# Kernel optimization log

Measured on AMD Instinct MI355X. Metric: run time of the kernel, lower is better.

Reference implementation:

```python
import jax, jax.numpy as jnp
import numpy as np

B, N, D, DS, LAT, FD, NF = 2, 384, 128, 3, 256, 1, 2
NPOS = DS * (2 * 5 + 1)  # 3 + 3*2*5 = 33
FREQS = np.linspace(1.0, 32.0, 5)  # torch.linspace(1, 2**5, 5)
EPS = 1e-5


def _bn(x, g, b):
    # BatchNorm1d, train-mode batch stats: normalize per channel over (batch, points)
    m = jnp.mean(x, axis=(0, 1))
    v = jnp.var(x, axis=(0, 1))
    return (x - m) * jax.lax.rsqrt(v + EPS) * g + b


def _tblock(xyz4, f, Wq, Wk, Wv, Wg1, bg1, Wg2, bg2, Wpe, bpe, g, b):
    # group_all=True full vector attention. f: [B,n,D], xyz4: [B,n,3]
    q = f @ Wq.T
    k = f @ Wk.T
    v = f @ Wv.T
    # knn_xyz gathered under no_grad in torch -> stop_gradient on the key side
    pd = xyz4[:, :, None] - jax.lax.stop_gradient(xyz4)[:, None]  # [B,n,n,3]
    parts = [pd]
    for fr in FREQS:
        parts.append(jnp.sin(pd * fr))
        parts.append(jnp.cos(pd * fr))
    pos = jnp.concatenate(parts, axis=-1) @ Wpe.T + bpe  # [B,n,n,D]
    edges = q[:, :, None] - k[:, None] + pos  # [B,n,n,D]
    h = jax.nn.relu(edges @ Wg1.T + bg1)
    attn = jax.nn.softmax(h @ Wg2.T + bg2, axis=-2)  # softmax over neighbor axis
    res = jnp.sum(attn * (v[:, None] + pos), axis=2)  # einsum bmnf,bmnf->bmf
    return _bn(res + f, g, b)


def setup_inputs() -> dict:
    key = jax.random.key(0)
    ks = iter(jax.random.split(key, 40))
    def rn(shape, s=0.05):
        return jax.random.normal(next(ks), shape, dtype=jnp.float32) * s
    z = lambda *s: jnp.zeros(s, jnp.float32)
    o = lambda *s: jnp.ones(s, jnp.float32)
    nb = NF + 1  # begin block + nfinal blocks
    return {
        "xyz": jax.random.normal(next(ks), (B, N, DS), dtype=jnp.float32),
        "feats": jax.random.normal(next(ks), (B, N, FD), dtype=jnp.float32),
        "enc_W": rn((D, FD)), "enc_b": z(D),
        "tb_Wq": rn((nb, D, D)), "tb_Wk": rn((nb, D, D)), "tb_Wv": rn((nb, D, D)),
        "tb_Wg1": rn((nb, D, D)), "tb_bg1": z(nb, D),
        "tb_Wg2": rn((nb, D, D)), "tb_bg2": z(nb, D),
        "tb_Wpe": rn((nb, D, NPOS)), "tb_bpe": z(nb, D),
        "tb_gamma": o(nb, D), "tb_beta": z(nb, D),
        "em_W1": rn((NF, D, D)), "em_b1": z(NF, D),
        "em_W2": rn((NF, D, D)), "em_b2": z(NF, D),
        "em_gamma": o(NF, D), "em_beta": z(NF, D),
        "fcf_W1": rn((LAT, D)), "fcf_b1": z(LAT),
        "fcf_W2": rn((LAT, LAT)), "fcf_b2": z(LAT),
    }


def reference(xyz, feats, enc_W, enc_b, tb_Wq, tb_Wk, tb_Wv, tb_Wg1, tb_bg1,
              tb_Wg2, tb_bg2, tb_Wpe, tb_bpe, tb_gamma, tb_beta,
              em_W1, em_b1, em_W2, em_b2, em_gamma, em_beta,
              fcf_W1, fcf_b1, fcf_W2, fcf_b2):
    f = feats @ enc_W.T + enc_b  # enc_feats
    x4 = xyz * 4.0
    for i in range(NF + 1):  # i=0: transformer_begin; i>=1: final transformers
        f = _tblock(x4, f, tb_Wq[i], tb_Wk[i], tb_Wv[i], tb_Wg1[i], tb_bg1[i],
                    tb_Wg2[i], tb_bg2[i], tb_Wpe[i], tb_bpe[i], tb_gamma[i], tb_beta[i])
        if i > 0:
            j = i - 1  # ElementwiseMLP: bn(x + relu(conv2(relu(conv1(x)))))
            y = jax.nn.relu(f @ em_W1[j].T + em_b1[j])
            y = jax.nn.relu(y @ em_W2[j].T + em_b2[j])
            f = _bn(f + y, em_gamma[j], em_beta[j])
    e = jax.nn.relu(f @ fcf_W1.T + fcf_b1) @ fcf_W2.T + fcf_b2
    return jnp.max(e, axis=1)  # lat_rep [B, lat_dim]
```

## Files before the change

### kernel.cpp

```cpp
#include <hip/hip_runtime.h>
#include <hip/hip_bf16.h>

#define B_ 2
#define N_ 384
#define D_ 128
#define LAT_ 256
#define NPOS_ 33
#define ROWS_ (B_*N_)
#define NT_ 64
#define ITERS_ (N_/NT_)

typedef __attribute__((ext_vector_type(8))) short bf16x8;
typedef __attribute__((ext_vector_type(4))) float f32x4;

#define MFMA(a,b,c) __builtin_amdgcn_mfma_f32_16x16x32_bf16((a),(b),(c),0,0,0)

__device__ __forceinline__ unsigned short f2bf(float x) {
    unsigned int u = __float_as_uint(x);
    u += 0x7FFFu + ((u >> 16) & 1u);
    return (unsigned short)(u >> 16);
}
__device__ __forceinline__ float bf2f(unsigned short u) {
    return __uint_as_float(((unsigned int)u) << 16);
}

__device__ __forceinline__ float bn_apply(float x, const float* stats, const float* gam,
                                          const float* bet, int d) {
    float s  = stats[d], sq = stats[128 + d];
    float mean = s * (1.f/ROWS_);
    float var  = sq * (1.f/ROWS_) - mean*mean;
    return (x - mean) * rsqrtf(var + 1e-5f) * gam[d] + bet[d];
}

#define PB_FPREP 192
#define PB_PSI   (PB_FPREP + 51)
#define PB_ENC   (PB_PSI + 384)
#define PB_WQG   (PB_ENC + 384)
__global__ __launch_bounds__(256) void prep_kernel(
    const float* __restrict__ xyz, const float* __restrict__ feats,
    const float* __restrict__ enc_W, const float* __restrict__ enc_b,
    const float* __restrict__ Wg1, const float* __restrict__ Wpe, const float* __restrict__ bpe,
    const float* __restrict__ Wq, const float* __restrict__ Wk,
    unsigned short* __restrict__ gF, float* __restrict__ psi,
    float* __restrict__ wqg, float* __restrict__ wkg, float* __restrict__ f)
{
    const int blk = blockIdx.x, t = threadIdx.x;
    if (blk < PB_FPREP) {
        int i = blk*256 + t;
        int n = i >> 6, q = i & 63;
        float val;
        if (q == 0) val = 1.f;
        else if (q < 4) val = 4.f*xyz[n*3 + (q-1)];
        else if (q < 34) {
            int u = q-4, fi = u/6, rem = u - fi*6, j = rem >> 1;
            const float fr = fi==0?1.f:(fi==1?8.75f:(fi==2?16.5f:(fi==3?24.25f:32.f)));
            float a = fr*4.f*xyz[n*3+j];
            val = (rem & 1) ? __sinf(a) : __cosf(a);
        } else val = 0.f;
        gF[n*64 + (q ^ ((n & 7) << 3))] = f2bf(val);
    } else if (blk < PB_PSI) {
        __shared__ float col2[2][D_];
        const int colid = (blk - PB_FPREP)*2 + (t >> 7);
        const int layer = colid / 34, p = colid - layer*34;
        const int e = t & 127, half = t >> 7;
        col2[half][e] = (p < NPOS_) ? Wpe[layer*D_*NPOS_ + e*NPOS_ + p]
                                    : bpe[layer*D_ + e];
        __syncthreads();
        const float* wg1 = Wg1 + layer*D_*D_;
        float acc = 0.f;
        #pragma unroll 4
        for (int d4 = 0; d4 < 32; ++d4) {
            float4 w = *(const float4*)(wg1 + e*D_ + d4*4);
            acc += w.x*col2[half][d4*4] + w.y*col2[half][d4*4+1]
                 + w.z*col2[half][d4*4+2] + w.w*col2[half][d4*4+3];
        }
        psi[layer*D_*34 + e*34 + p] = acc;
    } else if (blk < PB_ENC) {
        int i = (blk - PB_PSI)*256 + t;
        int r = i >> 7, d = i & 127;
        f[i] = feats[r]*enc_W[d] + enc_b[d];
    } else {
        __shared__ float col2[2][D_];
        const int colid = (blk - PB_ENC)*2 + (t >> 7);
        const int layer = colid >> 8, rem = colid & 255;
        const int mat = rem >> 7, ecol = rem & 127;
        const int e = t & 127, half = t >> 7;
        const float* Wsrc = mat ? Wk : Wq;
        col2[half][e] = Wsrc[layer*D_*D_ + e*D_ + ecol];
        __syncthreads();
        const float* wg1 = Wg1 + layer*D_*D_;
        float acc = 0.f;
        #pragma unroll 4
        for (int d4 = 0; d4 < 32; ++d4) {
            float4 w = *(const float4*)(wg1 + e*D_ + d4*4);
            acc += w.x*col2[half][d4*4] + w.y*col2[half][d4*4+1]
                 + w.z*col2[half][d4*4+2] + w.w*col2[half][d4*4+3];
        }
        float* dst = mat ? wkg : wqg;
        dst[layer*D_*D_ + e*D_ + ecol] = acc;
    }
}

__global__ __launch_bounds__(128) void qkv3_kernel(const float* __restrict__ graw,
    const float* __restrict__ stats, const float* __restrict__ gam, const float* __restrict__ bet,
    int use_stats,
    const float* __restrict__ Wv, const float* __restrict__ Wqg, const float* __restrict__ Wkg,
    const float* __restrict__ bg1,
    float* __restrict__ hb, unsigned short* __restrict__ kw16, unsigned short* __restrict__ v16)
{
    __shared__ float row[D_];
    const int r = blockIdx.x, d = threadIdx.x;
    float x = graw[r*D_ + d];
    if (use_stats) x = bn_apply(x, stats, gam, bet, d);
    row[d] = x;
    __syncthreads();
    float av = 0.f, ah = bg1[d], ak = 0.f;
    #pragma unroll 4
    for (int e4 = 0; e4 < D_/4; ++e4) {
        float4 wv = *(const float4*)(Wv  + d*D_ + e4*4);
        float4 wh = *(const float4*)(Wqg + d*D_ + e4*4);
        float4 wk = *(const float4*)(Wkg + d*D_ + e4*4);
        float4 xx = *(const float4*)&row[e4*4];
        av += wv.x*xx.x + wv.y*xx.y + wv.z*xx.z + wv.w*xx.w;
        ah += wh.x*xx.x + wh.y*xx.y + wh.z*xx.z + wh.w*xx.w;
        ak += wk.x*xx.x + wk.y*xx.y + wk.z*xx.z + wk.w*xx.w;
    }
    v16[r*D_ + d]  = f2bf(av);
    hb[r*D_ + d]   = ah;
    kw16[r*D_ + d] = f2bf(ak);
}

__global__ __launch_bounds__(512) void attn_mfma_kernel(
    const float* __restrict__ xyz, const float* __restrict__ graw,
    const float* __restrict__ stats_in, const float* __restrict__ gam_in,
    const float* __restrict__ bet_in, int use_stats,
    const float* __restrict__ hbb,
    const unsigned short* __restrict__ kwb, const unsigned short* __restrict__ vb,
    const unsigned short* __restrict__ gF,
    const float* __restrict__ psiL,
    const float* __restrict__ Wpe, const float* __restrict__ bpe,
    const float* __restrict__ Wg2, const float* __restrict__ bg2,
    float* __restrict__ gout, float* __restrict__ stats_out)
{
    __shared__ unsigned short sF[NT_*64];
    __shared__ unsigned short sH[NT_*128];
    __shared__ float sRed[4*128];

    const int t   = threadIdx.x;
    const int w   = t >> 6;
    const int l   = t & 63;
    const int lr  = l & 15;
    const int lg  = l >> 4;
    const int rb2 = w >> 2;
    const int ct0 = (w & 3) * 2;

    const int row  = blockIdx.x;
    const int b    = row / N_;
    const int brow = b * N_;

    uint4 freg = *(const uint4*)(gF + (size_t)brow*64 + t*8);
    unsigned short kw_us[2][2][4];
    unsigned short v_us[2][2][4];
    auto loadKW = [&](int n0) {
        #pragma unroll
        for (int rt = 0; rt < 2; ++rt)
        #pragma unroll
        for (int ct = 0; ct < 2; ++ct) {
            const int d = (ct0 + ct)*16 + lr;
            #pragma unroll
            for (int r = 0; r < 4; ++r) {
                const int rr = rb2*32 + rt*16 + lg*4 + r;
                kw_us[rt][ct][r] = kwb[(brow + n0 + rr)*D_ + d];
            }
        }
    };
    auto loadV = [&](int n0) {
        #pragma unroll
        for (int rt = 0; rt < 2; ++rt)
        #pragma unroll
        for (int ct = 0; ct < 2; ++ct) {
            const int d = (ct0 + ct)*16 + lr;
            #pragma unroll
            for (int r = 0; r < 4; ++r) {
                const int rr = rb2*32 + rt*16 + lg*4 + r;
                v_us[rt][ct][r] = vb[(brow + n0 + rr)*D_ + d];
            }
        }
    };
    loadKW(0);

    bf16x8 bWg2[2][4], bG[2][2], bT[2][2];
    float  hb_c[2], bg2_c[2];

    const float xm0 = 4.f*xyz[row*3+0];
    const float xm1 = 4.f*xyz[row*3+1];
    const float xm2 = 4.f*xyz[row*3+2];

    #pragma unroll
    for (int ct = 0; ct < 2; ++ct) {
        const int dout = (ct0 + ct) * 16 + lr;
        #pragma unroll
        for (int kt = 0; kt < 4; ++kt) {
            const float* p2 = Wg2 + dout * D_ + kt * 32 + lg * 8;
            float4 c0 = *(const float4*)(p2);
            float4 c1 = *(const float4*)(p2 + 4);
            bf16x8 v2;
            v2[0]=(short)f2bf(c0.x); v2[1]=(short)f2bf(c0.y); v2[2]=(short)f2bf(c0.z); v2[3]=(short)f2bf(c0.w);
            v2[4]=(short)f2bf(c1.x); v2[5]=(short)f2bf(c1.y); v2[6]=(short)f2bf(c1.z); v2[7]=(short)f2bf(c1.w);
            bWg2[ct][kt] = v2;
        }
        {
            const float* wrow = Wpe + dout*NPOS_;
            float bias = bpe[dout] + wrow[0]*xm0 + wrow[1]*xm1 + wrow[2]*xm2;
            #pragma unroll
            for (int kt = 0; kt < 2; ++kt) {
                bf16x8 g;
                #pragma unroll
                for (int e = 0; e < 8; ++e) {
                    const int qq = kt*32 + lg*8 + e;
                    float val;
                    if (qq == 0) val = bias;
                    else if (qq < 4) val = -wrow[qq-1];
                    else if (qq < 34) {
                        const int u = qq - 4, fi = u/6, rem = u - fi*6, j = rem >> 1;
                        const float Ws = wrow[3 + 6*fi + j];
                        const float Wc = wrow[3 + 6*fi + 3 + j];
                        const float fr = fi==0?1.f:(fi==1?8.75f:(fi==2?16.5f:(fi==3?24.25f:32.f)));
                        const float am = fr * (j==0?xm0:(j==1?xm1:xm2));
                        const float sm = __sinf(am), cm = __cosf(am);
                        val = (rem & 1) ? (Wc*sm - Ws*cm) : (Ws*sm + Wc*cm);
                    } else val = 0.f;
                    g[e] = (short)f2bf(val);
                }
                bG[ct][kt] = g;
            }
        }
        {
            const float* prow = psiL + dout*34;
            float bias = prow[33] + prow[0]*xm0 + prow[1]*xm1 + prow[2]*xm2;
            #pragma unroll
            for (int kt = 0; kt < 2; ++kt) {
                bf16x8 g;
                #pragma unroll
                for (int e = 0; e < 8; ++e) {
                    const int qq = kt*32 + lg*8 + e;
                    float val;
                    if (qq == 0) val = bias;
                    else if (qq < 4) val = -prow[qq-1];
                    else if (qq < 34) {
                        const int u = qq - 4, fi = u/6, rem = u - fi*6, j = rem >> 1;
                        const float Ws = prow[3 + 6*fi + j];
                        const float Wc = prow[3 + 6*fi + 3 + j];
                        const float fr = fi==0?1.f:(fi==1?8.75f:(fi==2?16.5f:(fi==3?24.25f:32.f)));
                        const float am = fr * (j==0?xm0:(j==1?xm1:xm2));
                        const float sm = __sinf(am), cm = __cosf(am);
                        val = (rem & 1) ? (Wc*sm - Ws*cm) : (Ws*sm + Wc*cm);
                    } else val = 0.f;
                    g[e] = (short)f2bf(val);
                }
                bT[ct][kt] = g;
            }
        }
        hb_c[ct]  = hbb[row*D_ + dout];
        bg2_c[ct] = bg2[dout];
    }

    *(uint4*)&sF[t*8] = freg;
    __syncthreads();

    float res_p[2] = {0.f, 0.f}, s_p[2] = {0.f, 0.f};
    f32x4 pos[2][2];

    for (int it = 0; it < ITERS_; ++it) {
        const int n0 = it * NT_;
        const bool more = (it < ITERS_ - 1);

        loadV(n0);
        if (more) freg = *(const uint4*)(gF + (size_t)(brow + n0 + NT_)*64 + t*8);
        f32x4 hacc[2][2];
        #pragma unroll
        for (int rt = 0; rt < 2; ++rt) {
            const int r16 = rb2*32 + rt*16 + lr;
            const int sw  = (r16 & 7) << 3;
            bf16x8 a0 = *(const bf16x8*)&sF[(r16*64 +  0 + lg*8) ^ sw];
            bf16x8 a1 = *(const bf16x8*)&sF[(r16*64 + 32 + lg*8) ^ sw];
            #pragma unroll
            for (int ct = 0; ct < 2; ++ct) {
                f32x4 z = {0.f,0.f,0.f,0.f};
                hacc[rt][ct] = MFMA(a1, bT[ct][1], MFMA(a0, bT[ct][0], z));
                pos[rt][ct]  = MFMA(a1, bG[ct][1], MFMA(a0, bG[ct][0], z));
            }
        }
        #pragma unroll
        for (int rt = 0; rt < 2; ++rt)
        #pragma unroll
        for (int ct = 0; ct < 2; ++ct) {
            const int d = (ct0 + ct)*16 + lr;
            #pragma unroll
            for (int r = 0; r < 4; ++r) {
                const int rr = rb2*32 + rt*16 + lg*4 + r;
                const float hv = hacc[rt][ct][r] + hb_c[ct] - bf2f(kw_us[rt][ct][r]);
                sH[(rr*128 + d) ^ ((rr & 7) << 3)] = f2bf(fmaxf(hv, 0.f));
            }
        }
        __syncthreads();

        if (more) {
            *(uint4*)&sF[t*8] = freg;
            loadKW(n0 + NT_);
        }
        f32x4 lacc[2][2];
        #pragma unroll
        for (int rt = 0; rt < 2; ++rt) {
            lacc[rt][0] = (f32x4){bg2_c[0], bg2_c[0], bg2_c[0], bg2_c[0]};
            lacc[rt][1] = (f32x4){bg2_c[1], bg2_c[1], bg2_c[1], bg2_c[1]};
            #pragma unroll
            for (int kt = 0; kt < 4; ++kt) {
                const int r16 = rb2*32 + rt*16 + lr;
                const int idx = (r16*128 + kt*32 + lg*8) ^ ((r16 & 7) << 3);
                bf16x8 a = *(const bf16x8*)&sH[idx];
                lacc[rt][0] = MFMA(a, bWg2[0][kt], lacc[rt][0]);
                lacc[rt][1] = MFMA(a, bWg2[1][kt], lacc[rt][1]);
            }
        }
        #pragma unroll
        for (int rt = 0; rt < 2; ++rt)
        #pragma unroll
        for (int ct = 0; ct < 2; ++ct) {
            #pragma unroll
            for (int r = 0; r < 4; ++r) {
                const float wgt = __expf(lacc[rt][ct][r]);
                const float vp  = bf2f(v_us[rt][ct][r]) + pos[rt][ct][r];
                res_p[ct] += wgt * vp;
                s_p[ct]   += wgt;
            }
        }
        __syncthreads();
    }

    #pragma unroll
    for (int ct = 0; ct < 2; ++ct) {
        #pragma unroll
        for (int off = 16; off < 64; off <<= 1) {
            res_p[ct] += __shfl_xor(res_p[ct], off, 64);
            s_p[ct]   += __shfl_xor(s_p[ct], off, 64);
        }
    }
    if (lg == 0) {
        #pragma unroll
        for (int ct = 0; ct < 2; ++ct) {
            const int d = (ct0 + ct)*16 + lr;
            sRed[(rb2*2+0)*128 + d] = res_p[ct];
            sRed[(rb2*2+1)*128 + d] = s_p[ct];
        }
    }
    __syncthreads();
    if (t < D_) {
        const float rsum = sRed[t]       + sRed[2*128 + t];
        const float ssum = sRed[128 + t] + sRed[3*128 + t];
        float fres = graw[row*D_ + t];
        if (use_stats) fres = bn_apply(fres, stats_in, gam_in, bet_in, t);
        const float val = rsum / ssum + fres;
        gout[row*D_ + t] = val;
        atomicAdd(&stats_out[t], val);
        atomicAdd(&stats_out[128 + t], val*val);
    }
}

__global__ __launch_bounds__(128) void em_kernel(const float* __restrict__ graw,
    const float* __restrict__ stats_in, const float* __restrict__ gam_in, const float* __restrict__ bet_in,
    const float* __restrict__ W1, const float* __restrict__ b1,
    const float* __restrict__ W2, const float* __restrict__ b2,
    float* __restrict__ gout, float* __restrict__ stats_out)
{
    __shared__ float row[D_], y1[D_];
    const int r = blockIdx.x, d = threadIdx.x;
    const float fn = bn_apply(graw[r*D_ + d], stats_in, gam_in, bet_in, d);
    row[d] = fn;
    __syncthreads();
    float a = b1[d];
    #pragma unroll 4
    for (int e4 = 0; e4 < D_/4; ++e4) {
        float4 w = *(const float4*)(W1 + d*D_ + e4*4);
        float4 x = *(const float4*)&row[e4*4];
        a += w.x*x.x + w.y*x.y + w.z*x.z + w.w*x.w;
    }
    y1[d] = fmaxf(a, 0.f);
    __syncthreads();
    float a2 = b2[d];
    #pragma unroll 4
    for (int e4 = 0; e4 < D_/4; ++e4) {
        float4 w = *(const float4*)(W2 + d*D_ + e4*4);
        float4 x = *(const float4*)&y1[e4*4];
        a2 += w.x*x.x + w.y*x.y + w.z*x.z + w.w*x.w;
    }
    const float g2 = fn + fmaxf(a2, 0.f);
    gout[r*D_ + d] = g2;
    atomicAdd(&stats_out[d], g2);
    atomicAdd(&stats_out[128 + d], g2*g2);
}

__global__ __launch_bounds__(256) void final_kernel(const float* __restrict__ graw,
    const float* __restrict__ stats_in, const float* __restrict__ gam_in, const float* __restrict__ bet_in,
    const float* __restrict__ W1, const float* __restrict__ b1,
    const float* __restrict__ W2, const float* __restrict__ b2,
    float* __restrict__ e_ws)
{
    __shared__ float rows[2][D_];
    __shared__ float h1[2][LAT_];
    const int r0 = blockIdx.x*2, t = threadIdx.x;
    {
        const int rr = t >> 7, d = t & 127;
        rows[rr][d] = bn_apply(graw[(r0+rr)*D_ + d], stats_in, gam_in, bet_in, d);
    }
    __syncthreads();
    float a[2] = {b1[t], b1[t]};
    #pragma unroll 4
    for (int e4 = 0; e4 < D_/4; ++e4) {
        float4 w = *(const float4*)(W1 + t*D_ + e4*4);
        #pragma unroll
        for (int rr = 0; rr < 2; ++rr) {
            float4 x = *(const float4*)&rows[rr][e4*4];
            a[rr] += w.x*x.x + w.y*x.y + w.z*x.z + w.w*x.w;
        }
    }
    #pragma unroll
    for (int rr = 0; rr < 2; ++rr) h1[rr][t] = fmaxf(a[rr], 0.f);
    __syncthreads();
    float a2[2] = {b2[t], b2[t]};
    #pragma unroll 4
    for (int e4 = 0; e4 < LAT_/4; ++e4) {
        float4 w = *(const float4*)(W2 + t*LAT_ + e4*4);
        #pragma unroll
        for (int rr = 0; rr < 2; ++rr) {
            float4 x = *(const float4*)&h1[rr][e4*4];
            a2[rr] += w.x*x.x + w.y*x.y + w.z*x.z + w.w*x.w;
        }
    }
    #pragma unroll
    for (int rr = 0; rr < 2; ++rr) e_ws[(r0+rr)*LAT_ + t] = a2[rr];
}

__global__ __launch_bounds__(256) void maxred_kernel(const float* __restrict__ e_ws,
                                                     float* __restrict__ out)
{
    int b = blockIdx.x, l = threadIdx.x;
    float m = -INFINITY;
    #pragma unroll 8
    for (int n=0;n<N_;n++) m = fmaxf(m, e_ws[(b*N_+n)*LAT_+l]);
    out[b*LAT_+l] = m;
}

extern "C" void kernel_launch(void* const* d_in, const int* in_sizes, int n_in,
                              void* d_out, int out_size, void* d_ws, size_t ws_size,
                              hipStream_t stream) {
    (void)in_sizes; (void)n_in; (void)out_size; (void)ws_size;
    const float* xyz    = (const float*)d_in[0];
    const float* feats  = (const float*)d_in[1];
    const float* enc_W  = (const float*)d_in[2];
    const float* enc_b  = (const float*)d_in[3];
    const float* tb_Wq  = (const float*)d_in[4];
    const float* tb_Wk  = (const float*)d_in[5];
    const float* tb_Wv  = (const float*)d_in[6];
    const float* tb_Wg1 = (const float*)d_in[7];
    const float* tb_bg1 = (const float*)d_in[8];
    const float* tb_Wg2 = (const float*)d_in[9];
    const float* tb_bg2 = (const float*)d_in[10];
    const float* tb_Wpe = (const float*)d_in[11];
    const float* tb_bpe = (const float*)d_in[12];
    const float* tb_gamma = (const float*)d_in[13];
    const float* tb_beta  = (const float*)d_in[14];
    const float* em_W1  = (const float*)d_in[15];
    const float* em_b1  = (const float*)d_in[16];
    const float* em_W2  = (const float*)d_in[17];
    const float* em_b2  = (const float*)d_in[18];
    const float* em_gamma = (const float*)d_in[19];
    const float* em_beta  = (const float*)d_in[20];
    const float* fcf_W1 = (const float*)d_in[21];
    const float* fcf_b1 = (const float*)d_in[22];
    const float* fcf_W2 = (const float*)d_in[23];
    const float* fcf_b2 = (const float*)d_in[24];
    float* out = (float*)d_out;

    float* ws   = (float*)d_ws;
    float* buf0 = ws;
    float* buf1 = buf0 + ROWS_*D_;
    float* hbb  = buf1 + ROWS_*D_;
    float* ebuf = hbb  + ROWS_*D_;
    float* psi  = ebuf + ROWS_*LAT_;
    float* wqg  = psi  + 3*D_*34;
    float* wkg  = wqg  + 3*D_*D_;
    float* stats = wkg + 3*D_*D_;
    float* sA0 = stats;
    float* sA1 = stats + 256;
    float* sE1 = stats + 512;
    float* sA2 = stats + 768;
    float* sE2 = stats + 1024;
    unsigned short* kwbuf = (unsigned short*)(stats + 5*256);
    unsigned short* vbuf  = kwbuf + ROWS_*D_;
    unsigned short* gF    = vbuf + ROWS_*D_;

    hipMemsetAsync(stats, 0, 5*256*sizeof(float), stream);

    prep_kernel<<<PB_WQG, 256, 0, stream>>>(xyz, feats, enc_W, enc_b,
        tb_Wg1, tb_Wpe, tb_bpe, tb_Wq, tb_Wk, gF, psi, wqg, wkg, buf0);

    const float* gz = tb_gamma;
    qkv3_kernel<<<ROWS_, 128, 0, stream>>>(buf0, gz, gz, gz, 0,
        tb_Wv, wqg, wkg, tb_bg1, hbb, kwbuf, vbuf);
    attn_mfma_kernel<<<ROWS_, 512, 0, stream>>>(xyz, buf0, gz, gz, gz, 0,
        hbb, kwbuf, vbuf, gF, psi,
        tb_Wpe, tb_bpe, tb_Wg2, tb_bg2, buf1, sA0);
    qkv3_kernel<<<ROWS_, 128, 0, stream>>>(buf1, sA0, tb_gamma, tb_beta, 1,
        tb_Wv + 1*D_*D_, wqg + 1*D_*D_, wkg + 1*D_*D_, tb_bg1 + 1*D_, hbb, kwbuf, vbuf);
    attn_mfma_kernel<<<ROWS_, 512, 0, stream>>>(xyz, buf1, sA0, tb_gamma, tb_beta, 1,
        hbb, kwbuf, vbuf, gF, psi + 1*D_*34,
        tb_Wpe + 1*D_*NPOS_, tb_bpe + 1*D_, tb_Wg2 + 1*D_*D_, tb_bg2 + 1*D_, buf0, sA1);
    em_kernel<<<ROWS_, 128, 0, stream>>>(buf0, sA1, tb_gamma + 1*D_, tb_beta + 1*D_,
                                         em_W1, em_b1, em_W2, em_b2, buf1, sE1);
    qkv3_kernel<<<ROWS_, 128, 0, stream>>>(buf1, sE1, em_gamma, em_beta, 1,
        tb_Wv + 2*D_*D_, wqg + 2*D_*D_, wkg + 2*D_*D_, tb_bg1 + 2*D_, hbb, kwbuf, vbuf);
    attn_mfma_kernel<<<ROWS_, 512, 0, stream>>>(xyz, buf1, sE1, em_gamma, em_beta, 1,
        hbb, kwbuf, vbuf, gF, psi + 2*D_*34,
        tb_Wpe + 2*D_*NPOS_, tb_bpe + 2*D_, tb_Wg2 + 2*D_*D_, tb_bg2 + 2*D_, buf0, sA2);
    em_kernel<<<ROWS_, 128, 0, stream>>>(buf0, sA2, tb_gamma + 2*D_, tb_beta + 2*D_,
                                         em_W1 + 1*D_*D_, em_b1 + 1*D_,
                                         em_W2 + 1*D_*D_, em_b2 + 1*D_, buf1, sE2);
    final_kernel<<<ROWS_/2, 256, 0, stream>>>(buf1, sE2, em_gamma + 1*D_, em_beta + 1*D_,
                                              fcf_W1, fcf_b1, fcf_W2, fcf_b2, ebuf);
    maxred_kernel<<<B_, 256, 0, stream>>>(ebuf, out);
}
```

Measured before the change: 572.6 us.

## Stage K/V tiles through transposed LDS and batch four rows per em block

The attention kernel now loads K and V tiles with coalesced 32-bit global loads into padded, transposed shared-memory buffers, replacing per-lane scattered 16-bit global loads. It prefetches the next tile during compute and adds an extra barrier per iteration. It also raises wave priority around the MFMA sections. The elementwise MLP kernel now handles four rows per block so each weight load is reused across rows, which cuts the grid size by four. The extra LDS use (about 33KB) may lower occupancy, and the added barrier costs synchronisation time.

```diff
diff --git a/kernel.cpp b/kernel.cpp
--- a/kernel.cpp
+++ b/kernel.cpp
@@ -144,6 +144,8 @@
 {
     __shared__ unsigned short sF[NT_*64];
     __shared__ unsigned short sH[NT_*128];
+    __shared__ unsigned short sKW[D_*66];
+    __shared__ unsigned short sV[D_*66];
     __shared__ float sRed[4*128];
 
     const int t   = threadIdx.x;
@@ -158,36 +160,33 @@
     const int b    = row / N_;
     const int brow = b * N_;
 
+    const unsigned int* sKW32 = (const unsigned int*)sKW;
+    const unsigned int* sV32  = (const unsigned int*)sV;
+
+    unsigned int kvK[8], kvV[8];
+    const int st_rr0 = t >> 6;
+    const int st_dd  = (t & 63) * 2;
+    auto issueKV = [&](int n0) {
+        #pragma unroll
+        for (int p = 0; p < 8; ++p) {
+            const int g = (brow + n0 + p*8 + st_rr0)*D_ + st_dd;
+            kvK[p] = *(const unsigned int*)(kwb + g);
+            kvV[p] = *(const unsigned int*)(vb + g);
+        }
+    };
+    auto writeKV = [&]() {
+        #pragma unroll
+        for (int p = 0; p < 8; ++p) {
+            const int rr = p*8 + st_rr0;
+            sKW[st_dd*66 + rr]     = (unsigned short)(kvK[p] & 0xffffu);
+            sKW[(st_dd+1)*66 + rr] = (unsigned short)(kvK[p] >> 16);
+            sV [st_dd*66 + rr]     = (unsigned short)(kvV[p] & 0xffffu);
+            sV [(st_dd+1)*66 + rr] = (unsigned short)(kvV[p] >> 16);
+        }
+    };
+
+    issueKV(0);
     uint4 freg = *(const uint4*)(gF + (size_t)brow*64 + t*8);
-    unsigned short kw_us[2][2][4];
-    unsigned short v_us[2][2][4];
-    auto loadKW = [&](int n0) {
-        #pragma unroll
-        for (int rt = 0; rt < 2; ++rt)
-        #pragma unroll
-        for (int ct = 0; ct < 2; ++ct) {
-            const int d = (ct0 + ct)*16 + lr;
-            #pragma unroll
-            for (int r = 0; r < 4; ++r) {
-                const int rr = rb2*32 + rt*16 + lg*4 + r;
-                kw_us[rt][ct][r] = kwb[(brow + n0 + rr)*D_ + d];
-            }
-        }
-    };
-    auto loadV = [&](int n0) {
-        #pragma unroll
-        for (int rt = 0; rt < 2; ++rt)
-        #pragma unroll
-        for (int ct = 0; ct < 2; ++ct) {
-            const int d = (ct0 + ct)*16 + lr;
-            #pragma unroll
-            for (int r = 0; r < 4; ++r) {
-                const int rr = rb2*32 + rt*16 + lg*4 + r;
-                v_us[rt][ct][r] = vb[(brow + n0 + rr)*D_ + d];
-            }
-        }
-    };
-    loadKW(0);
 
     bf16x8 bWg2[2][4], bG[2][2], bT[2][2];
     float  hb_c[2], bg2_c[2];
@@ -265,6 +264,7 @@
         bg2_c[ct] = bg2[dout];
     }
 
+    writeKV();
     *(uint4*)&sF[t*8] = freg;
     __syncthreads();
 
@@ -272,12 +272,12 @@
     f32x4 pos[2][2];
 
     for (int it = 0; it < ITERS_; ++it) {
+        const bool more = (it < ITERS_ - 1);
         const int n0 = it * NT_;
-        const bool more = (it < ITERS_ - 1);
-
-        loadV(n0);
-        if (more) freg = *(const uint4*)(gF + (size_t)(brow + n0 + NT_)*64 + t*8);
+        (void)n0;
+
         f32x4 hacc[2][2];
+        __builtin_amdgcn_s_setprio(1);
         #pragma unroll
         for (int rt = 0; rt < 2; ++rt) {
             const int r16 = rb2*32 + rt*16 + lr;
@@ -291,25 +291,34 @@
                 pos[rt][ct]  = MFMA(a1, bG[ct][1], MFMA(a0, bG[ct][0], z));
             }
         }
+        __builtin_amdgcn_s_setprio(0);
         #pragma unroll
         for (int rt = 0; rt < 2; ++rt)
         #pragma unroll
         for (int ct = 0; ct < 2; ++ct) {
-            const int d = (ct0 + ct)*16 + lr;
+            const int d  = (ct0 + ct)*16 + lr;
+            const int rr = rb2*32 + rt*16 + lg*4;
+            const unsigned int a01 = sKW32[d*33 + (rr >> 1)];
+            const unsigned int a23 = sKW32[d*33 + (rr >> 1) + 1];
+            float kv[4];
+            kv[0] = __uint_as_float(a01 << 16);
+            kv[1] = __uint_as_float(a01 & 0xffff0000u);
+            kv[2] = __uint_as_float(a23 << 16);
+            kv[3] = __uint_as_float(a23 & 0xffff0000u);
             #pragma unroll
             for (int r = 0; r < 4; ++r) {
-                const int rr = rb2*32 + rt*16 + lg*4 + r;
-                const float hv = hacc[rt][ct][r] + hb_c[ct] - bf2f(kw_us[rt][ct][r]);
-                sH[(rr*128 + d) ^ ((rr & 7) << 3)] = f2bf(fmaxf(hv, 0.f));
+                const float hv = hacc[rt][ct][r] + hb_c[ct] - kv[r];
+                sH[((rr + r)*128 + d) ^ (((rr + r) & 7) << 3)] = f2bf(fmaxf(hv, 0.f));
             }
         }
         __syncthreads();
 
         if (more) {
-            *(uint4*)&sF[t*8] = freg;
-            loadKW(n0 + NT_);
+            issueKV(n0 + NT_);
+            freg = *(const uint4*)(gF + (size_t)(brow + n0 + NT_)*64 + t*8);
         }
         f32x4 lacc[2][2];
+        __builtin_amdgcn_s_setprio(1);
         #pragma unroll
         for (int rt = 0; rt < 2; ++rt) {
             lacc[rt][0] = (f32x4){bg2_c[0], bg2_c[0], bg2_c[0], bg2_c[0]};
@@ -323,19 +332,34 @@
                 lacc[rt][1] = MFMA(a, bWg2[1][kt], lacc[rt][1]);
             }
         }
+        __builtin_amdgcn_s_setprio(0);
         #pragma unroll
         for (int rt = 0; rt < 2; ++rt)
         #pragma unroll
         for (int ct = 0; ct < 2; ++ct) {
+            const int d  = (ct0 + ct)*16 + lr;
+            const int rr = rb2*32 + rt*16 + lg*4;
+            const unsigned int a01 = sV32[d*33 + (rr >> 1)];
+            const unsigned int a23 = sV32[d*33 + (rr >> 1) + 1];
+            float vv[4];
+            vv[0] = __uint_as_float(a01 << 16);
+            vv[1] = __uint_as_float(a01 & 0xffff0000u);
+            vv[2] = __uint_as_float(a23 << 16);
+            vv[3] = __uint_as_float(a23 & 0xffff0000u);
             #pragma unroll
             for (int r = 0; r < 4; ++r) {
                 const float wgt = __expf(lacc[rt][ct][r]);
-                const float vp  = bf2f(v_us[rt][ct][r]) + pos[rt][ct][r];
-                res_p[ct] += wgt * vp;
+                res_p[ct] += wgt * (vv[r] + pos[rt][ct][r]);
                 s_p[ct]   += wgt;
             }
         }
         __syncthreads();
+
+        if (more) {
+            writeKV();
+            *(uint4*)&sF[t*8] = freg;
+            __syncthreads();
+        }
     }
 
     #pragma unroll
@@ -373,31 +397,45 @@
     const float* __restrict__ W2, const float* __restrict__ b2,
     float* __restrict__ gout, float* __restrict__ stats_out)
 {
-    __shared__ float row[D_], y1[D_];
-    const int r = blockIdx.x, d = threadIdx.x;
-    const float fn = bn_apply(graw[r*D_ + d], stats_in, gam_in, bet_in, d);
-    row[d] = fn;
-    __syncthreads();
-    float a = b1[d];
+    __shared__ float rows[4][D_], y1[4][D_];
+    const int r0 = blockIdx.x*4, d = threadIdx.x;
+    float fn[4];
+    #pragma unroll
+    for (int rr = 0; rr < 4; ++rr) {
+        fn[rr] = bn_apply(graw[(r0+rr)*D_ + d], stats_in, gam_in, bet_in, d);
+        rows[rr][d] = fn[rr];
+    }
+    __syncthreads();
+    float a[4] = {b1[d], b1[d], b1[d], b1[d]};
     #pragma unroll 4
     for (int e4 = 0; e4 < D_/4; ++e4) {
         float4 w = *(const float4*)(W1 + d*D_ + e4*4);
-        float4 x = *(const float4*)&row[e4*4];
-        a += w.x*x.x + w.y*x.y + w.z*x.z + w.w*x.w;
-    }
-    y1[d] = fmaxf(a, 0.f);
-    __syncthreads();
-    float a2 = b2[d];
+        #pragma unroll
+        for (int rr = 0; rr < 4; ++rr) {
+            float4 x = *(const float4*)&rows[rr][e4*4];
+            a[rr] += w.x*x.x + w.y*x.y + w.z*x.z + w.w*x.w;
+        }
+    }
+    #pragma unroll
+    for (int rr = 0; rr < 4; ++rr) y1[rr][d] = fmaxf(a[rr], 0.f);
+    __syncthreads();
+    float a2[4] = {b2[d], b2[d], b2[d], b2[d]};
     #pragma unroll 4
     for (int e4 = 0; e4 < D_/4; ++e4) {
         float4 w = *(const float4*)(W2 + d*D_ + e4*4);
-        float4 x = *(const float4*)&y1[e4*4];
-        a2 += w.x*x.x + w.y*x.y + w.z*x.z + w.w*x.w;
-    }
-    const float g2 = fn + fmaxf(a2, 0.f);
-    gout[r*D_ + d] = g2;
-    atomicAdd(&stats_out[d], g2);
-    atomicAdd(&stats_out[128 + d], g2*g2);
+        #pragma unroll
+        for (int rr = 0; rr < 4; ++rr) {
+            float4 x = *(const float4*)&y1[rr][e4*4];
+            a2[rr] += w.x*x.x + w.y*x.y + w.z*x.z + w.w*x.w;
+        }
+    }
+    #pragma unroll
+    for (int rr = 0; rr < 4; ++rr) {
+        const float g2 = fn[rr] + fmaxf(a2[rr], 0.f);
+        gout[(r0+rr)*D_ + d] = g2;
+        atomicAdd(&stats_out[d], g2);
+        atomicAdd(&stats_out[128+d], g2*g2);
+    }
 }
 
 __global__ __launch_bounds__(256) void final_kernel(const float* __restrict__ graw,
@@ -516,16 +554,16 @@
     attn_mfma_kernel<<<ROWS_, 512, 0, stream>>>(xyz, buf1, sA0, tb_gamma, tb_beta, 1,
         hbb, kwbuf, vbuf, gF, psi + 1*D_*34,
         tb_Wpe + 1*D_*NPOS_, tb_bpe + 1*D_, tb_Wg2 + 1*D_*D_, tb_bg2 + 1*D_, buf0, sA1);
-    em_kernel<<<ROWS_, 128, 0, stream>>>(buf0, sA1, tb_gamma + 1*D_, tb_beta + 1*D_,
-                                         em_W1, em_b1, em_W2, em_b2, buf1, sE1);
+    em_kernel<<<ROWS_/4, 128, 0, stream>>>(buf0, sA1, tb_gamma + 1*D_, tb_beta + 1*D_,
+                                           em_W1, em_b1, em_W2, em_b2, buf1, sE1);
     qkv3_kernel<<<ROWS_, 128, 0, stream>>>(buf1, sE1, em_gamma, em_beta, 1,
         tb_Wv + 2*D_*D_, wqg + 2*D_*D_, wkg + 2*D_*D_, tb_bg1 + 2*D_, hbb, kwbuf, vbuf);
     attn_mfma_kernel<<<ROWS_, 512, 0, stream>>>(xyz, buf1, sE1, em_gamma, em_beta, 1,
         hbb, kwbuf, vbuf, gF, psi + 2*D_*34,
         tb_Wpe + 2*D_*NPOS_, tb_bpe + 2*D_, tb_Wg2 + 2*D_*D_, tb_bg2 + 2*D_, buf0, sA2);
-    em_kernel<<<ROWS_, 128, 0, stream>>>(buf0, sA2, tb_gamma + 2*D_, tb_beta + 2*D_,
-                                         em_W1 + 1*D_*D_, em_b1 + 1*D_,
-                                         em_W2 + 1*D_*D_, em_b2 + 1*D_, buf1, sE2);
+    em_kernel<<<ROWS_/4, 128, 0, stream>>>(buf0, sA2, tb_gamma + 2*D_, tb_beta + 2*D_,
+                                           em_W1 + 1*D_*D_, em_b1 + 1*D_,
+                                           em_W2 + 1*D_*D_, em_b2 + 1*D_, buf1, sE2);
     final_kernel<<<ROWS_/2, 256, 0, stream>>>(buf1, sE2, em_gamma + 1*D_, em_beta + 1*D_,
                                               fcf_W1, fcf_b1, fcf_W2, fcf_b2, ebuf);
     maxred_kernel<<<B_, 256, 0, stream>>>(ebuf, out);
```

New measurement: 579.8 us. About the same (+1.3%).
